# Kernel tuning notes

Hardware: AMD Instinct MI355X
Metric: run time of the kernel (lower is better)

Reference implementation:

```python
import jax, jax.numpy as jnp
import numpy as np

HIDDEN = 256

def _segment_mean(src, seg_ids, num_segments):
    # scatter_mean with count clamped to min 1 (matches torch reference)
    s = jax.ops.segment_sum(src, seg_ids, num_segments=num_segments)
    cnt = jax.ops.segment_sum(jnp.ones((src.shape[0],), src.dtype), seg_ids,
                              num_segments=num_segments)
    return s / jnp.maximum(cnt, 1.0)[:, None]


def setup_inputs() -> dict:
    key = jax.random.key(0)
    ks = jax.random.split(key, 12)
    N, E = 25000, 400000
    F_NODE, F_EDGE, F_OUT = 128, 128, 128
    x = jax.random.normal(ks[0], (N, F_NODE), jnp.float32)
    edge_index = jax.random.randint(ks[1], (2, E), 0, N, jnp.int64)
    edge_attr = jax.random.normal(ks[2], (E, F_EDGE), jnp.float32)
    u = jax.random.normal(ks[3], (1, 64), jnp.float32)
    batch = jnp.zeros((N,), jnp.int64)
    s1 = 1.0 / np.sqrt(F_NODE + F_EDGE)
    s2 = 1.0 / np.sqrt(HIDDEN)
    s3 = 1.0 / np.sqrt(F_NODE + HIDDEN)
    # node_mlp_1: Linear(256,256) -> ELU -> Linear(256,256)
    W1a = jax.random.uniform(ks[4], (F_NODE + F_EDGE, HIDDEN), jnp.float32, -s1, s1)
    b1a = jax.random.uniform(ks[5], (HIDDEN,), jnp.float32, -s1, s1)
    W1b = jax.random.uniform(ks[6], (HIDDEN, HIDDEN), jnp.float32, -s2, s2)
    b1b = jax.random.uniform(ks[7], (HIDDEN,), jnp.float32, -s2, s2)
    # node_mlp_2: Linear(384,256) -> ELU -> Linear(256,128)
    W2a = jax.random.uniform(ks[8], (F_NODE + HIDDEN, HIDDEN), jnp.float32, -s3, s3)
    b2a = jax.random.uniform(ks[9], (HIDDEN,), jnp.float32, -s3, s3)
    W2b = jax.random.uniform(ks[10], (HIDDEN, F_OUT), jnp.float32, -s2, s2)
    b2b = jax.random.uniform(ks[11], (F_OUT,), jnp.float32, -s2, s2)
    return {"x": x, "edge_index": edge_index, "edge_attr": edge_attr, "u": u,
            "batch": batch, "W1a": W1a, "b1a": b1a, "W1b": W1b, "b1b": b1b,
            "W2a": W2a, "b2a": b2a, "W2b": W2b, "b2b": b2b}


def reference(x, edge_index, edge_attr, u, batch,
              W1a, b1a, W1b, b1b, W2a, b2a, W2b, b2b):
    row, col = edge_index[0], edge_index[1]
    # gather source node feats per edge, concat with edge feats: [E, 256]
    h = jnp.concatenate([x[row], edge_attr], axis=1)
    # node_mlp_1
    h = jax.nn.elu(h @ W1a + b1a) @ W1b + b1b          # [E, 256]
    # scatter_mean onto destination nodes
    agg = _segment_mean(h, col, x.shape[0])             # [N, 256]
    # node_mlp_2 on [x, agg]
    z = jnp.concatenate([x, agg], axis=1)               # [N, 384]
    return jax.nn.elu(z @ W2a + b2a) @ W2b + b2b        # [N, 128]
```

## Files before the change

kernel.cpp:

```cpp
#include <hip/hip_runtime.h>
#include <hip/hip_bf16.h>
#include <stdint.h>

typedef short short8 __attribute__((ext_vector_type(8)));
typedef float f32x4 __attribute__((ext_vector_type(4)));
typedef float fvec4 __attribute__((ext_vector_type(4)));
typedef unsigned short us4 __attribute__((ext_vector_type(4)));

static __device__ __forceinline__ unsigned short f2bf(float f) {
  return __bfloat16_as_ushort(__float2bfloat16(f));
}

static __device__ __forceinline__ float bf2f(unsigned short u) {
  union { uint32_t u; float f; } v; v.u = (uint32_t)u << 16;
  return v.f;
}

static __device__ __forceinline__ float elu_f(float v) {
  return v > 0.0f ? v : __expf(v) - 1.0f;
}

__global__ void prep_kernel(const float* __restrict__ W1a, const float* __restrict__ W1b,
                            const float* __restrict__ W2a, const float* __restrict__ W2b,
                            unsigned short* __restrict__ w1aP, unsigned short* __restrict__ w1bP,
                            unsigned short* __restrict__ w2aP, unsigned short* __restrict__ w2bP,
                            const int* __restrict__ col_idx, int* __restrict__ cnt, int E,
                            float* __restrict__ agg, int aggN, int hb) {
  int b = blockIdx.x;
  if (b < 1024) {
    int p = b * 256 + threadIdx.x;
    const float* W; unsigned short* dst; int KT, Nc, q;
    if (p < 65536)       { W = W1a; dst = w1aP; KT = 8;  Nc = 256; q = p; }
    else if (p < 131072) { W = W1b; dst = w1bP; KT = 8;  Nc = 256; q = p - 65536; }
    else if (p < 229376) { W = W2a; dst = w2aP; KT = 12; Nc = 256; q = p - 131072; }
    else                 { W = W2b; dst = w2bP; KT = 8;  Nc = 128; q = p - 229376; }
    int i = q & 7;
    int l = (q >> 3) & 63;
    int rest = q >> 9;
    int kt = rest % KT;
    int nt = rest / KT;
    dst[q] = f2bf(W[(size_t)(kt * 32 + (l >> 4) * 8 + i) * Nc + nt * 16 + (l & 15)]);
  } else if (b < 1024 + hb) {
    int i = (b - 1024) * 256 + threadIdx.x;
    if (i < E) atomicAdd(&cnt[col_idx[i]], 1);
  } else {
    int idx = (b - 1024 - hb) * 256 + threadIdx.x;
    if (idx * 4 < aggN) {
      fvec4 z = {0.f, 0.f, 0.f, 0.f};
      *(fvec4*)(agg + (size_t)idx * 4) = z;
    }
  }
}

__global__ __launch_bounds__(1024) void scan_kernel(const int* __restrict__ cnt,
                                                    int* __restrict__ startA,
                                                    int* __restrict__ offs, int N, int E) {
  __shared__ int partial[1024];
  const int t = threadIdx.x;
  const int chunk = (N + 1023) >> 10;
  const int base = t * chunk;
  int s = 0;
  for (int i = 0; i < chunk; ++i) {
    int idx = base + i;
    if (idx < N) s += cnt[idx];
  }
  partial[t] = s;
  __syncthreads();
  for (int o = 1; o < 1024; o <<= 1) {
    int a = (t >= o) ? partial[t - o] : 0;
    __syncthreads();
    partial[t] += a;
    __syncthreads();
  }
  int run = partial[t] - s;
  for (int i = 0; i < chunk; ++i) {
    int idx = base + i;
    if (idx < N) {
      startA[idx] = run;
      offs[idx] = run;
      run += cnt[idx];
    }
  }
  if (t == 0) startA[N] = E;
}

__global__ void eid_kernel(const int* __restrict__ col_idx, int* __restrict__ offs,
                           int* __restrict__ eid, int E) {
  int i = blockIdx.x * blockDim.x + threadIdx.x;
  if (i < E) eid[atomicAdd(&offs[col_idx[i]], 1)] = i;
}

#define LDA 264
#define EBR 32

__global__ __launch_bounds__(256, 6) void edge_mlp_kernel(
    const float* __restrict__ x, const int* __restrict__ row_idx,
    const int* __restrict__ col_idx, const float* __restrict__ eattr,
    const float* __restrict__ b1a,
    const unsigned short* __restrict__ w1aP,
    const int* __restrict__ eid, float* __restrict__ agg) {
  __shared__ __align__(16) unsigned short As[EBR * LDA];
  __shared__ int rowi[EBR];
  __shared__ int eidx[EBR];
  __shared__ int dsts[EBR];
  const int t = threadIdx.x;
  const int e0 = blockIdx.x * EBR;

  if (t < EBR) {
    int e = eid[e0 + t];
    eidx[t] = e;
    rowi[t] = row_idx[e];
    dsts[t] = col_idx[e];
  }

  const int w = t >> 6, l = t & 63;
  const int lr = l & 15, lk = l >> 4;
  const unsigned short* B1 = w1aP + (size_t)(w * 32) * 512 + (size_t)l * 8;

  short8 bA[4], bB[4];
#pragma unroll
  for (int n = 0; n < 4; ++n) bA[n] = *(const short8*)(B1 + n * 4096);

  __syncthreads();

  for (int idx = t; idx < EBR * 64; idx += 256) {
    int e = idx >> 6, c4 = idx & 63;
    fvec4 v;
    if (c4 < 32)
      v = *(const fvec4*)(x + (size_t)rowi[e] * 128 + c4 * 4);
    else
      v = __builtin_nontemporal_load((const fvec4*)(eattr + (size_t)eidx[e] * 128 + (c4 - 32) * 4));
    us4 o;
    o.x = f2bf(v.x); o.y = f2bf(v.y); o.z = f2bf(v.z); o.w = f2bf(v.w);
    *(us4*)(&As[e * LDA + c4 * 4]) = o;
  }
  __syncthreads();

  f32x4 acc[2][4];
  const f32x4 zero4 = {0.f, 0.f, 0.f, 0.f};
#pragma unroll
  for (int mt = 0; mt < 2; ++mt)
#pragma unroll
    for (int nt = 0; nt < 4; ++nt) acc[mt][nt] = zero4;

#pragma unroll
  for (int kt = 0; kt < 8; ++kt) {
    short8* bc = (kt & 1) ? bB : bA;
    short8* bn = (kt & 1) ? bA : bB;
    if (kt < 7) {
#pragma unroll
      for (int n = 0; n < 4; ++n) bn[n] = *(const short8*)(B1 + n * 4096 + (kt + 1) * 512);
    }
    short8 a[2];
#pragma unroll
    for (int mt = 0; mt < 2; ++mt)
      a[mt] = *(const short8*)(&As[(mt * 16 + lr) * LDA + kt * 32 + lk * 8]);
#pragma unroll
    for (int mt = 0; mt < 2; ++mt)
#pragma unroll
      for (int nt = 0; nt < 4; ++nt)
        acc[mt][nt] = __builtin_amdgcn_mfma_f32_16x16x32_bf16(a[mt], bc[nt], acc[mt][nt], 0, 0, 0);
  }
  __syncthreads();

#pragma unroll
  for (int nt = 0; nt < 4; ++nt) {
    int col = w * 64 + nt * 16 + lr;
    float bias = b1a[col];
#pragma unroll
    for (int mt = 0; mt < 2; ++mt)
#pragma unroll
      for (int j = 0; j < 4; ++j) {
        float v = elu_f(acc[mt][nt][j] + bias);
        As[(mt * 16 + lk * 4 + j) * LDA + col] = f2bf(v);
      }
  }
  __syncthreads();

  {
    const int col = t;
    float run = 0.f;
    int prev = dsts[0];
    int segstart = 0;
#pragma unroll 8
    for (int r = 0; r < EBR; ++r) {
      int d = dsts[r];
      if (d != prev) {
        if (segstart == 0)
          atomicAdd(&agg[(size_t)prev * 256 + col], run);
        else
          agg[(size_t)prev * 256 + col] = run;
        run = 0.f;
        prev = d;
        segstart = r;
      }
      run += bf2f(As[r * LDA + col]);
    }
    atomicAdd(&agg[(size_t)prev * 256 + col], run);
  }
}

#define LDN 392

__global__ __launch_bounds__(256, 3) void node_mlp_kernel(
    const float* __restrict__ x, const float* __restrict__ agg,
    const int* __restrict__ startA, const float* __restrict__ b1b,
    const float* __restrict__ b2a, const float* __restrict__ b2b,
    const unsigned short* __restrict__ w1bP, const unsigned short* __restrict__ w2aP,
    const unsigned short* __restrict__ w2bP,
    float* __restrict__ out, int N) {
  __shared__ __align__(16) unsigned short As[64 * LDN];
  __shared__ float inv64[64];
  const int t = threadIdx.x;
  const int n0 = blockIdx.x * 64;

  const int w = t >> 6, l = t & 63;
  const int lr = l & 15, lk = l >> 4;
  const unsigned short* B0 = w1bP + (size_t)(w * 32) * 512 + (size_t)l * 8;
  const unsigned short* B1 = w2aP + (size_t)(w * 48) * 512 + (size_t)l * 8;
  const unsigned short* B2 = w2bP + (size_t)(w * 16) * 512 + (size_t)l * 8;

  if (t < 64) {
    int node = n0 + t;
    int cn = (node < N) ? (startA[node + 1] - startA[node]) : 0;
    inv64[t] = cn > 0 ? 1.0f / (float)cn : 0.f;
  }

  short8 bA[4], bB[4];
#pragma unroll
  for (int n = 0; n < 4; ++n) bA[n] = *(const short8*)(B0 + n * 4096);

  __syncthreads();

  for (int idx = t; idx < 64 * 64; idx += 256) {
    int nn = idx >> 6, c4 = idx & 63;
    int node = n0 + nn;
    fvec4 v = {0.f, 0.f, 0.f, 0.f};
    if (node < N) {
      float inv = inv64[nn];
      fvec4 a = *(const fvec4*)(agg + (size_t)node * 256 + c4 * 4);
      v.x = a.x * inv; v.y = a.y * inv; v.z = a.z * inv; v.w = a.w * inv;
    }
    us4 o;
    o.x = f2bf(v.x); o.y = f2bf(v.y); o.z = f2bf(v.z); o.w = f2bf(v.w);
    *(us4*)(&As[nn * 264 + c4 * 4]) = o;
  }
  __syncthreads();

  const f32x4 zero4 = {0.f, 0.f, 0.f, 0.f};
  f32x4 accU[4][4];
#pragma unroll
  for (int mt = 0; mt < 4; ++mt)
#pragma unroll
    for (int nt = 0; nt < 4; ++nt) accU[mt][nt] = zero4;

#pragma unroll
  for (int kt = 0; kt < 8; ++kt) {
    short8* bc = (kt & 1) ? bB : bA;
    short8* bn = (kt & 1) ? bA : bB;
    if (kt < 7) {
#pragma unroll
      for (int n = 0; n < 4; ++n) bn[n] = *(const short8*)(B0 + n * 4096 + (kt + 1) * 512);
    }
    short8 a[4];
#pragma unroll
    for (int mt = 0; mt < 4; ++mt)
      a[mt] = *(const short8*)(&As[(mt * 16 + lr) * 264 + kt * 32 + lk * 8]);
#pragma unroll
    for (int mt = 0; mt < 4; ++mt)
#pragma unroll
      for (int nt = 0; nt < 4; ++nt)
        accU[mt][nt] = __builtin_amdgcn_mfma_f32_16x16x32_bf16(a[mt], bc[nt], accU[mt][nt], 0, 0, 0);
  }

#pragma unroll
  for (int n = 0; n < 4; ++n) bA[n] = *(const short8*)(B1 + n * 6144);

  __syncthreads();

  for (int idx = t; idx < 64 * 32; idx += 256) {
    int nn = idx >> 5, c4 = idx & 31;
    int node = n0 + nn;
    fvec4 v = {0.f, 0.f, 0.f, 0.f};
    if (node < N) v = *(const fvec4*)(x + (size_t)node * 128 + c4 * 4);
    us4 o;
    o.x = f2bf(v.x); o.y = f2bf(v.y); o.z = f2bf(v.z); o.w = f2bf(v.w);
    *(us4*)(&As[nn * LDN + c4 * 4]) = o;
  }

#pragma unroll
  for (int nt = 0; nt < 4; ++nt) {
    int col = w * 64 + nt * 16 + lr;
    float bias = b1b[col];
#pragma unroll
    for (int mt = 0; mt < 4; ++mt)
#pragma unroll
      for (int j = 0; j < 4; ++j) {
        int row = mt * 16 + lk * 4 + j;
        float g = inv64[row] > 0.f ? 1.f : 0.f;
        As[row * LDN + 128 + col] = f2bf(accU[mt][nt][j] + g * bias);
      }
  }
  __syncthreads();

  f32x4 acc[4][4];
#pragma unroll
  for (int mt = 0; mt < 4; ++mt)
#pragma unroll
    for (int nt = 0; nt < 4; ++nt) acc[mt][nt] = zero4;

#pragma unroll
  for (int kt = 0; kt < 12; ++kt) {
    short8* bc = (kt & 1) ? bB : bA;
    short8* bn = (kt & 1) ? bA : bB;
    if (kt < 11) {
#pragma unroll
      for (int n = 0; n < 4; ++n) bn[n] = *(const short8*)(B1 + n * 6144 + (kt + 1) * 512);
    }
    short8 a[4];
#pragma unroll
    for (int mt = 0; mt < 4; ++mt)
      a[mt] = *(const short8*)(&As[(mt * 16 + lr) * LDN + kt * 32 + lk * 8]);
#pragma unroll
    for (int mt = 0; mt < 4; ++mt)
#pragma unroll
      for (int nt = 0; nt < 4; ++nt)
        acc[mt][nt] = __builtin_amdgcn_mfma_f32_16x16x32_bf16(a[mt], bc[nt], acc[mt][nt], 0, 0, 0);
  }

#pragma unroll
  for (int n = 0; n < 2; ++n) bA[n] = *(const short8*)(B2 + n * 4096);

  __syncthreads();

#pragma unroll
  for (int nt = 0; nt < 4; ++nt) {
    int col = w * 64 + nt * 16 + lr;
    float bias = b2a[col];
#pragma unroll
    for (int mt = 0; mt < 4; ++mt)
#pragma unroll
      for (int j = 0; j < 4; ++j) {
        float v = elu_f(acc[mt][nt][j] + bias);
        As[(mt * 16 + lk * 4 + j) * 264 + col] = f2bf(v);
      }
  }
  __syncthreads();

  f32x4 acc2[4][2];
#pragma unroll
  for (int mt = 0; mt < 4; ++mt)
#pragma unroll
    for (int nt = 0; nt < 2; ++nt) acc2[mt][nt] = zero4;
#pragma unroll
  for (int kt = 0; kt < 8; ++kt) {
    short8* bc = (kt & 1) ? bB : bA;
    short8* bn = (kt & 1) ? bA : bB;
    if (kt < 7) {
#pragma unroll
      for (int n = 0; n < 2; ++n) bn[n] = *(const short8*)(B2 + n * 4096 + (kt + 1) * 512);
    }
    short8 a[4];
#pragma unroll
    for (int mt = 0; mt < 4; ++mt)
      a[mt] = *(const short8*)(&As[(mt * 16 + lr) * 264 + kt * 32 + lk * 8]);
#pragma unroll
    for (int mt = 0; mt < 4; ++mt)
#pragma unroll
      for (int nt = 0; nt < 2; ++nt)
        acc2[mt][nt] = __builtin_amdgcn_mfma_f32_16x16x32_bf16(a[mt], bc[nt], acc2[mt][nt], 0, 0, 0);
  }

#pragma unroll
  for (int nt = 0; nt < 2; ++nt) {
    int col = w * 32 + nt * 16 + lr;
    float bias = b2b[col];
#pragma unroll
    for (int mt = 0; mt < 4; ++mt)
#pragma unroll
      for (int j = 0; j < 4; ++j) {
        int node = n0 + mt * 16 + lk * 4 + j;
        if (node < N) out[(size_t)node * 128 + col] = acc2[mt][nt][j] + bias;
      }
  }
}

extern "C" void kernel_launch(void* const* d_in, const int* in_sizes, int n_in,
                              void* d_out, int out_size, void* d_ws, size_t ws_size,
                              hipStream_t stream) {
  const float* x = (const float*)d_in[0];
  const int* ei = (const int*)d_in[1];
  const float* eattr = (const float*)d_in[2];
  const float* W1a = (const float*)d_in[5];
  const float* b1a = (const float*)d_in[6];
  const float* W1b = (const float*)d_in[7];
  const float* b1b = (const float*)d_in[8];
  const float* W2a = (const float*)d_in[9];
  const float* b2a = (const float*)d_in[10];
  const float* W2b = (const float*)d_in[11];
  const float* b2b = (const float*)d_in[12];

  const int N = in_sizes[0] / 128;
  const int E = in_sizes[2] / 128;

  char* ws = (char*)d_ws;
  float* agg = (float*)ws;
  size_t off = (size_t)N * 256 * 4;
  int* cntbuf = (int*)(ws + off); off += (size_t)N * 4;
  int* startA = (int*)(ws + off); off += (size_t)(N + 1) * 4;
  int* offs   = (int*)(ws + off); off += (size_t)N * 4;
  int* eid    = (int*)(ws + off); off += (size_t)E * 4;
  off = (off + 255) & ~(size_t)255;
  unsigned short* w1aP = (unsigned short*)(ws + off); off += 256 * 256 * 2;
  unsigned short* w1bP = (unsigned short*)(ws + off); off += 256 * 256 * 2;
  unsigned short* w2aP = (unsigned short*)(ws + off); off += 384 * 256 * 2;
  unsigned short* w2bP = (unsigned short*)(ws + off);

  (void)hipMemsetAsync(cntbuf, 0, (size_t)N * 4, stream);

  const int hb = (E + 255) / 256;
  const int aggN = N * 256;
  const int zb = (aggN / 4 + 255) / 256;

  prep_kernel<<<1024 + hb + zb, 256, 0, stream>>>(
      W1a, W1b, W2a, W2b, w1aP, w1bP, w2aP, w2bP, ei + E, cntbuf, E, agg, aggN, hb);

  scan_kernel<<<1, 1024, 0, stream>>>(cntbuf, startA, offs, N, E);
  eid_kernel<<<hb, 256, 0, stream>>>(ei + E, offs, eid, E);

  edge_mlp_kernel<<<E / EBR, 256, 0, stream>>>(x, ei, ei + E, eattr, b1a, w1aP, eid, agg);

  node_mlp_kernel<<<(N + 63) / 64, 256, 0, stream>>>(x, agg, startA, b1b, b2a, b2b,
                                                     w1bP, w2aP, w2bP, (float*)d_out, N);
}
```

Before: 260.8 us.

## Pre-sort edge attributes to bf16 in CSR order and pre-convert x to bf16

The eid permutation kernel is replaced by a scatter kernel that writes row/dst indices and bf16-converted edge attributes directly into destination-sorted order. x is converted to bf16 once in the prep kernel. The edge MLP then reads contiguous bf16 edge rows and half-size x rows with no conversion and no eid indirection. The cost is an extra full write and read of a bf16 copy of edge_attr (about 100MB) in exchange for a random fp32 gather that no longer has to happen inside the MLP kernel.

```diff
diff --git a/kernel.cpp b/kernel.cpp
--- a/kernel.cpp
+++ b/kernel.cpp
@@ -6,6 +6,7 @@
 typedef float f32x4 __attribute__((ext_vector_type(4)));
 typedef float fvec4 __attribute__((ext_vector_type(4)));
 typedef unsigned short us4 __attribute__((ext_vector_type(4)));
+typedef unsigned short us8 __attribute__((ext_vector_type(8)));
 
 static __device__ __forceinline__ unsigned short f2bf(float f) {
   return __bfloat16_as_ushort(__float2bfloat16(f));
@@ -25,7 +26,9 @@
                             unsigned short* __restrict__ w1aP, unsigned short* __restrict__ w1bP,
                             unsigned short* __restrict__ w2aP, unsigned short* __restrict__ w2bP,
                             const int* __restrict__ col_idx, int* __restrict__ cnt, int E,
-                            float* __restrict__ agg, int aggN, int hb) {
+                            float* __restrict__ agg, int aggN, int hb, int zb,
+                            const float* __restrict__ x, unsigned short* __restrict__ xH,
+                            int xElems) {
   int b = blockIdx.x;
   if (b < 1024) {
     int p = b * 256 + threadIdx.x;
@@ -43,11 +46,22 @@
   } else if (b < 1024 + hb) {
     int i = (b - 1024) * 256 + threadIdx.x;
     if (i < E) atomicAdd(&cnt[col_idx[i]], 1);
-  } else {
+  } else if (b < 1024 + hb + zb) {
     int idx = (b - 1024 - hb) * 256 + threadIdx.x;
     if (idx * 4 < aggN) {
       fvec4 z = {0.f, 0.f, 0.f, 0.f};
       *(fvec4*)(agg + (size_t)idx * 4) = z;
+    }
+  } else {
+    int idx = (b - 1024 - hb - zb) * 256 + threadIdx.x;
+    if (idx * 8 < xElems) {
+      const float* src = x + (size_t)idx * 8;
+      fvec4 a = *(const fvec4*)src;
+      fvec4 c = *(const fvec4*)(src + 4);
+      us8 o;
+      o[0] = f2bf(a.x); o[1] = f2bf(a.y); o[2] = f2bf(a.z); o[3] = f2bf(a.w);
+      o[4] = f2bf(c.x); o[5] = f2bf(c.y); o[6] = f2bf(c.z); o[7] = f2bf(c.w);
+      *(us8*)(xH + (size_t)idx * 8) = o;
     }
   }
 }
@@ -84,33 +98,54 @@
   if (t == 0) startA[N] = E;
 }
 
-__global__ void eid_kernel(const int* __restrict__ col_idx, int* __restrict__ offs,
-                           int* __restrict__ eid, int E) {
-  int i = blockIdx.x * blockDim.x + threadIdx.x;
-  if (i < E) eid[atomicAdd(&offs[col_idx[i]], 1)] = i;
+__global__ __launch_bounds__(256) void scatter_kernel(
+    const int* __restrict__ row_idx, const int* __restrict__ col_idx,
+    const float* __restrict__ eattr, int* __restrict__ offs,
+    int* __restrict__ rowS, int* __restrict__ dstS,
+    unsigned short* __restrict__ eattrS, int E) {
+  __shared__ int rr[64];
+  const int t = threadIdx.x;
+  const int e0 = blockIdx.x * 64;
+
+  if (t < 64) {
+    int e = e0 + t;
+    int d = col_idx[e];
+    int r = atomicAdd(&offs[d], 1);
+    rr[t] = r;
+    rowS[r] = row_idx[e];
+    dstS[r] = d;
+  }
+  __syncthreads();
+
+  for (int idx = t; idx < 64 * 16; idx += 256) {
+    int e = idx >> 4, c = idx & 15;
+    const fvec4* src = (const fvec4*)(eattr + (size_t)(e0 + e) * 128 + c * 8);
+    fvec4 a = __builtin_nontemporal_load(src);
+    fvec4 b = __builtin_nontemporal_load(src + 1);
+    us8 o;
+    o[0] = f2bf(a.x); o[1] = f2bf(a.y); o[2] = f2bf(a.z); o[3] = f2bf(a.w);
+    o[4] = f2bf(b.x); o[5] = f2bf(b.y); o[6] = f2bf(b.z); o[7] = f2bf(b.w);
+    *(us8*)(eattrS + (size_t)rr[e] * 128 + c * 8) = o;
+  }
 }
 
 #define LDA 264
 #define EBR 32
 
 __global__ __launch_bounds__(256, 6) void edge_mlp_kernel(
-    const float* __restrict__ x, const int* __restrict__ row_idx,
-    const int* __restrict__ col_idx, const float* __restrict__ eattr,
-    const float* __restrict__ b1a,
-    const unsigned short* __restrict__ w1aP,
-    const int* __restrict__ eid, float* __restrict__ agg) {
+    const unsigned short* __restrict__ xH, const int* __restrict__ rowS,
+    const int* __restrict__ dstS, const unsigned short* __restrict__ eattrS,
+    const float* __restrict__ b1a, const unsigned short* __restrict__ w1aP,
+    float* __restrict__ agg) {
   __shared__ __align__(16) unsigned short As[EBR * LDA];
   __shared__ int rowi[EBR];
-  __shared__ int eidx[EBR];
   __shared__ int dsts[EBR];
   const int t = threadIdx.x;
   const int e0 = blockIdx.x * EBR;
 
   if (t < EBR) {
-    int e = eid[e0 + t];
-    eidx[t] = e;
-    rowi[t] = row_idx[e];
-    dsts[t] = col_idx[e];
+    rowi[t] = rowS[e0 + t];
+    dsts[t] = dstS[e0 + t];
   }
 
   const int w = t >> 6, l = t & 63;
@@ -123,16 +158,14 @@
 
   __syncthreads();
 
-  for (int idx = t; idx < EBR * 64; idx += 256) {
-    int e = idx >> 6, c4 = idx & 63;
-    fvec4 v;
-    if (c4 < 32)
-      v = *(const fvec4*)(x + (size_t)rowi[e] * 128 + c4 * 4);
+  for (int idx = t; idx < EBR * 32; idx += 256) {
+    int e = idx >> 5, g = idx & 31;
+    us8 v;
+    if (g < 16)
+      v = *(const us8*)(xH + (size_t)rowi[e] * 128 + g * 8);
     else
-      v = __builtin_nontemporal_load((const fvec4*)(eattr + (size_t)eidx[e] * 128 + (c4 - 32) * 4));
-    us4 o;
-    o.x = f2bf(v.x); o.y = f2bf(v.y); o.z = f2bf(v.z); o.w = f2bf(v.w);
-    *(us4*)(&As[e * LDA + c4 * 4]) = o;
+      v = *(const us8*)(eattrS + (size_t)(e0 + e) * 128 + (g - 16) * 8);
+    *(us8*)(&As[e * LDA + g * 8]) = v;
   }
   __syncthreads();
 
@@ -409,8 +442,12 @@
   int* cntbuf = (int*)(ws + off); off += (size_t)N * 4;
   int* startA = (int*)(ws + off); off += (size_t)(N + 1) * 4;
   int* offs   = (int*)(ws + off); off += (size_t)N * 4;
-  int* eid    = (int*)(ws + off); off += (size_t)E * 4;
+  int* rowS   = (int*)(ws + off); off += (size_t)E * 4;
+  int* dstS   = (int*)(ws + off); off += (size_t)E * 4;
   off = (off + 255) & ~(size_t)255;
+  unsigned short* xH     = (unsigned short*)(ws + off); off += (size_t)N * 128 * 2;
+  off = (off + 255) & ~(size_t)255;
+  unsigned short* eattrS = (unsigned short*)(ws + off); off += (size_t)E * 128 * 2;
   unsigned short* w1aP = (unsigned short*)(ws + off); off += 256 * 256 * 2;
   unsigned short* w1bP = (unsigned short*)(ws + off); off += 256 * 256 * 2;
   unsigned short* w2aP = (unsigned short*)(ws + off); off += 384 * 256 * 2;
@@ -421,14 +458,19 @@
   const int hb = (E + 255) / 256;
   const int aggN = N * 256;
   const int zb = (aggN / 4 + 255) / 256;
-
-  prep_kernel<<<1024 + hb + zb, 256, 0, stream>>>(
-      W1a, W1b, W2a, W2b, w1aP, w1bP, w2aP, w2bP, ei + E, cntbuf, E, agg, aggN, hb);
+  const int xElems = N * 128;
+  const int xb = (xElems / 8 + 255) / 256;
+
+  prep_kernel<<<1024 + hb + zb + xb, 256, 0, stream>>>(
+      W1a, W1b, W2a, W2b, w1aP, w1bP, w2aP, w2bP, ei + E, cntbuf, E,
+      agg, aggN, hb, zb, x, xH, xElems);
 
   scan_kernel<<<1, 1024, 0, stream>>>(cntbuf, startA, offs, N, E);
-  eid_kernel<<<hb, 256, 0, stream>>>(ei + E, offs, eid, E);
-
-  edge_mlp_kernel<<<E / EBR, 256, 0, stream>>>(x, ei, ei + E, eattr, b1a, w1aP, eid, agg);
+
+  scatter_kernel<<<E / 64, 256, 0, stream>>>(ei, ei + E, eattr, offs,
+                                             rowS, dstS, eattrS, E);
+
+  edge_mlp_kernel<<<E / EBR, 256, 0, stream>>>(xH, rowS, dstS, eattrS, b1a, w1aP, agg);
 
   node_mlp_kernel<<<(N + 63) / 64, 256, 0, stream>>>(x, agg, startA, b1b, b2a, b2b,
                                                      w1bP, w2aP, w2bP, (float*)d_out, N);
```

Result: slower. 279.7 us (+7.3%).

## Fuse edge MLP, segment mean and node MLP into one node-tiled kernel

Applied to the files above, without the earlier changes.

Replaces the separate edge-MLP and node-MLP kernels with one kernel in which each block owns 32 destination nodes and walks their CSR-sorted incoming edges in chunks. Segment sums accumulate in LDS rather than through global atomics into an fp32 agg buffer, which removes the agg zeroing, the atomics and the agg round trip through global memory. x is converted to bf16 once in the prep kernel so the gathers read half as many bytes. The trade-off is imbalance: blocks whose nodes have many incoming edges take longer. Larger LDS use per block and the smaller node tile for the node MLP can also lower occupancy and weight reuse.

```diff
diff --git a/kernel.cpp b/kernel.cpp
--- a/kernel.cpp
+++ b/kernel.cpp
@@ -6,6 +6,7 @@
 typedef float f32x4 __attribute__((ext_vector_type(4)));
 typedef float fvec4 __attribute__((ext_vector_type(4)));
 typedef unsigned short us4 __attribute__((ext_vector_type(4)));
+typedef unsigned short us8 __attribute__((ext_vector_type(8)));
 
 static __device__ __forceinline__ unsigned short f2bf(float f) {
   return __bfloat16_as_ushort(__float2bfloat16(f));
@@ -25,7 +26,8 @@
                             unsigned short* __restrict__ w1aP, unsigned short* __restrict__ w1bP,
                             unsigned short* __restrict__ w2aP, unsigned short* __restrict__ w2bP,
                             const int* __restrict__ col_idx, int* __restrict__ cnt, int E,
-                            float* __restrict__ agg, int aggN, int hb) {
+                            int hb, const float* __restrict__ x,
+                            unsigned short* __restrict__ xH, int xElems) {
   int b = blockIdx.x;
   if (b < 1024) {
     int p = b * 256 + threadIdx.x;
@@ -45,9 +47,14 @@
     if (i < E) atomicAdd(&cnt[col_idx[i]], 1);
   } else {
     int idx = (b - 1024 - hb) * 256 + threadIdx.x;
-    if (idx * 4 < aggN) {
-      fvec4 z = {0.f, 0.f, 0.f, 0.f};
-      *(fvec4*)(agg + (size_t)idx * 4) = z;
+    if (idx * 8 < xElems) {
+      const float* src = x + (size_t)idx * 8;
+      fvec4 a = *(const fvec4*)src;
+      fvec4 c = *(const fvec4*)(src + 4);
+      us8 o;
+      o[0] = f2bf(a.x); o[1] = f2bf(a.y); o[2] = f2bf(a.z); o[3] = f2bf(a.w);
+      o[4] = f2bf(c.x); o[5] = f2bf(c.y); o[6] = f2bf(c.z); o[7] = f2bf(c.w);
+      *(us8*)(xH + (size_t)idx * 8) = o;
     }
   }
 }
@@ -91,82 +98,237 @@
 }
 
 #define LDA 264
-#define EBR 32
-
-__global__ __launch_bounds__(256, 6) void edge_mlp_kernel(
-    const float* __restrict__ x, const int* __restrict__ row_idx,
-    const int* __restrict__ col_idx, const float* __restrict__ eattr,
-    const float* __restrict__ b1a,
-    const unsigned short* __restrict__ w1aP,
-    const int* __restrict__ eid, float* __restrict__ agg) {
-  __shared__ __align__(16) unsigned short As[EBR * LDA];
-  __shared__ int rowi[EBR];
-  __shared__ int eidx[EBR];
-  __shared__ int dsts[EBR];
+#define LDX 392
+#define LDC 260
+#define NBF 32
+
+__global__ __launch_bounds__(256, 3) void fused_kernel(
+    const unsigned short* __restrict__ xH, const int* __restrict__ eid,
+    const int* __restrict__ row_idx, const float* __restrict__ eattr,
+    const int* __restrict__ startA,
+    const float* __restrict__ b1a, const float* __restrict__ b1b,
+    const float* __restrict__ b2a, const float* __restrict__ b2b,
+    const unsigned short* __restrict__ w1aP, const unsigned short* __restrict__ w1bP,
+    const unsigned short* __restrict__ w2aP, const unsigned short* __restrict__ w2bP,
+    float* __restrict__ out, int N) {
+  __shared__ __align__(16) float accumS[NBF * LDC];
+  __shared__ __align__(16) unsigned short As[NBF * LDA];
+  __shared__ int startL[NBF + 1];
+  __shared__ int eidL[NBF], rowiL[NBF], nodeL[NBF];
+  __shared__ float invL[NBF];
+
   const int t = threadIdx.x;
-  const int e0 = blockIdx.x * EBR;
-
-  if (t < EBR) {
-    int e = eid[e0 + t];
-    eidx[t] = e;
-    rowi[t] = row_idx[e];
-    dsts[t] = col_idx[e];
-  }
-
+  const int n0 = blockIdx.x * NBF;
   const int w = t >> 6, l = t & 63;
   const int lr = l & 15, lk = l >> 4;
-  const unsigned short* B1 = w1aP + (size_t)(w * 32) * 512 + (size_t)l * 8;
-
+
+  if (t < NBF + 1) startL[t] = startA[min(n0 + t, N)];
+  for (int idx = t; idx < NBF * 256; idx += 256)
+    accumS[(idx >> 8) * LDC + (idx & 255)] = 0.f;
+  __syncthreads();
+  if (t < NBF) {
+    int cn = startL[t + 1] - startL[t];
+    invL[t] = cn > 0 ? 1.0f / (float)cn : 0.f;
+  }
+  const int sBase = startL[0], sEnd = startL[NBF];
+
+  const unsigned short* B1w = w1aP + (size_t)(w * 32) * 512 + (size_t)l * 8;
   short8 bA[4], bB[4];
-#pragma unroll
-  for (int n = 0; n < 4; ++n) bA[n] = *(const short8*)(B1 + n * 4096);
-
-  __syncthreads();
-
-  for (int idx = t; idx < EBR * 64; idx += 256) {
-    int e = idx >> 6, c4 = idx & 63;
-    fvec4 v;
-    if (c4 < 32)
-      v = *(const fvec4*)(x + (size_t)rowi[e] * 128 + c4 * 4);
-    else
-      v = __builtin_nontemporal_load((const fvec4*)(eattr + (size_t)eidx[e] * 128 + (c4 - 32) * 4));
-    us4 o;
-    o.x = f2bf(v.x); o.y = f2bf(v.y); o.z = f2bf(v.z); o.w = f2bf(v.w);
-    *(us4*)(&As[e * LDA + c4 * 4]) = o;
-  }
-  __syncthreads();
-
   f32x4 acc[2][4];
   const f32x4 zero4 = {0.f, 0.f, 0.f, 0.f};
+
+  float biasA[4];
+#pragma unroll
+  for (int nt = 0; nt < 4; ++nt) biasA[nt] = b1a[w * 64 + nt * 16 + lr];
+
+  for (int s = sBase; s < sEnd; s += NBF) {
+    __syncthreads();
+    if (t < NBF) {
+      int slot = s + t;
+      int sl = slot < sEnd ? slot : sEnd - 1;
+      int e = eid[sl];
+      eidL[t] = e;
+      rowiL[t] = row_idx[e];
+      int lo = 0;
+#pragma unroll
+      for (int st = 16; st > 0; st >>= 1)
+        if (lo + st <= NBF - 1 && startL[lo + st] <= sl) lo += st;
+      nodeL[t] = lo;
+    }
+#pragma unroll
+    for (int n = 0; n < 4; ++n) bA[n] = *(const short8*)(B1w + n * 4096);
+    __syncthreads();
+
+    for (int idx = t; idx < NBF * 32; idx += 256) {
+      int r = idx >> 5, g = idx & 31;
+      us8 v;
+      if (g < 16) {
+        v = *(const us8*)(xH + (size_t)rowiL[r] * 128 + g * 8);
+      } else {
+        const fvec4* src = (const fvec4*)(eattr + (size_t)eidL[r] * 128 + (size_t)(g - 16) * 8);
+        fvec4 a = __builtin_nontemporal_load(src);
+        fvec4 b = __builtin_nontemporal_load(src + 1);
+        v[0] = f2bf(a.x); v[1] = f2bf(a.y); v[2] = f2bf(a.z); v[3] = f2bf(a.w);
+        v[4] = f2bf(b.x); v[5] = f2bf(b.y); v[6] = f2bf(b.z); v[7] = f2bf(b.w);
+      }
+      *(us8*)(&As[r * LDA + g * 8]) = v;
+    }
+    __syncthreads();
+
+#pragma unroll
+    for (int mt = 0; mt < 2; ++mt)
+#pragma unroll
+      for (int nt = 0; nt < 4; ++nt) acc[mt][nt] = zero4;
+#pragma unroll
+    for (int kt = 0; kt < 8; ++kt) {
+      short8* bc = (kt & 1) ? bB : bA;
+      short8* bn = (kt & 1) ? bA : bB;
+      if (kt < 7) {
+#pragma unroll
+        for (int n = 0; n < 4; ++n) bn[n] = *(const short8*)(B1w + n * 4096 + (kt + 1) * 512);
+      }
+      short8 a[2];
+#pragma unroll
+      for (int mt = 0; mt < 2; ++mt)
+        a[mt] = *(const short8*)(&As[(mt * 16 + lr) * LDA + kt * 32 + lk * 8]);
+#pragma unroll
+      for (int mt = 0; mt < 2; ++mt)
+#pragma unroll
+        for (int nt = 0; nt < 4; ++nt)
+          acc[mt][nt] = __builtin_amdgcn_mfma_f32_16x16x32_bf16(a[mt], bc[nt], acc[mt][nt], 0, 0, 0);
+    }
+    __syncthreads();
+
+#pragma unroll
+    for (int nt = 0; nt < 4; ++nt) {
+      int col = w * 64 + nt * 16 + lr;
+#pragma unroll
+      for (int mt = 0; mt < 2; ++mt)
+#pragma unroll
+        for (int j = 0; j < 4; ++j) {
+          float v = elu_f(acc[mt][nt][j] + biasA[nt]);
+          As[(mt * 16 + lk * 4 + j) * LDA + col] = f2bf(v);
+        }
+    }
+    __syncthreads();
+
+    {
+      int c = sEnd - s; if (c > NBF) c = NBF;
+      const int col = t;
+      float run = 0.f;
+      int prev = nodeL[0];
+      for (int r = 0; r < c; ++r) {
+        int nd = nodeL[r];
+        if (nd != prev) { accumS[prev * LDC + col] += run; run = 0.f; prev = nd; }
+        run += bf2f(As[r * LDA + col]);
+      }
+      accumS[prev * LDC + col] += run;
+    }
+  }
+  __syncthreads();
+
+  const unsigned short* B0  = w1bP + (size_t)(w * 32) * 512 + (size_t)l * 8;
+  const unsigned short* B1n = w2aP + (size_t)(w * 48) * 512 + (size_t)l * 8;
+  const unsigned short* B2n = w2bP + (size_t)(w * 16) * 512 + (size_t)l * 8;
+
+#pragma unroll
+  for (int n = 0; n < 4; ++n) bA[n] = *(const short8*)(B0 + n * 4096);
+
+  for (int idx = t; idx < NBF * 64; idx += 256) {
+    int nn = idx >> 6, c4 = idx & 63;
+    float inv = invL[nn];
+    const float* a = &accumS[nn * LDC + c4 * 4];
+    us4 o;
+    o.x = f2bf(a[0] * inv); o.y = f2bf(a[1] * inv);
+    o.z = f2bf(a[2] * inv); o.w = f2bf(a[3] * inv);
+    *(us4*)(&As[nn * LDA + c4 * 4]) = o;
+  }
+  __syncthreads();
+
+  f32x4 accU[2][4];
 #pragma unroll
   for (int mt = 0; mt < 2; ++mt)
 #pragma unroll
-    for (int nt = 0; nt < 4; ++nt) acc[mt][nt] = zero4;
-
+    for (int nt = 0; nt < 4; ++nt) accU[mt][nt] = zero4;
 #pragma unroll
   for (int kt = 0; kt < 8; ++kt) {
     short8* bc = (kt & 1) ? bB : bA;
     short8* bn = (kt & 1) ? bA : bB;
     if (kt < 7) {
 #pragma unroll
-      for (int n = 0; n < 4; ++n) bn[n] = *(const short8*)(B1 + n * 4096 + (kt + 1) * 512);
+      for (int n = 0; n < 4; ++n) bn[n] = *(const short8*)(B0 + n * 4096 + (kt + 1) * 512);
     }
     short8 a[2];
 #pragma unroll
     for (int mt = 0; mt < 2; ++mt)
       a[mt] = *(const short8*)(&As[(mt * 16 + lr) * LDA + kt * 32 + lk * 8]);
+#pragma unroll
+    for (int mt = 0; mt < 2; ++mt)
+#pragma unroll
+      for (int nt = 0; nt < 4; ++nt)
+        accU[mt][nt] = __builtin_amdgcn_mfma_f32_16x16x32_bf16(a[mt], bc[nt], accU[mt][nt], 0, 0, 0);
+  }
+
+  unsigned short* XB = (unsigned short*)accumS;
+
+  for (int idx = t; idx < NBF * 16; idx += 256) {
+    int nn = idx >> 4, g = idx & 15;
+    int node = n0 + nn;
+    us8 v = {0, 0, 0, 0, 0, 0, 0, 0};
+    if (node < N) v = *(const us8*)(xH + (size_t)node * 128 + g * 8);
+    *(us8*)(&XB[nn * LDX + g * 8]) = v;
+  }
+
+#pragma unroll
+  for (int n = 0; n < 4; ++n) bA[n] = *(const short8*)(B1n + n * 6144);
+
+#pragma unroll
+  for (int nt = 0; nt < 4; ++nt) {
+    int col = w * 64 + nt * 16 + lr;
+    float bias = b1b[col];
+#pragma unroll
+    for (int mt = 0; mt < 2; ++mt)
+#pragma unroll
+      for (int j = 0; j < 4; ++j) {
+        int row = mt * 16 + lk * 4 + j;
+        float g = invL[row] > 0.f ? 1.f : 0.f;
+        XB[row * LDX + 128 + col] = f2bf(accU[mt][nt][j] + g * bias);
+      }
+  }
+  __syncthreads();
+
+#pragma unroll
+  for (int mt = 0; mt < 2; ++mt)
+#pragma unroll
+    for (int nt = 0; nt < 4; ++nt) acc[mt][nt] = zero4;
+#pragma unroll
+  for (int kt = 0; kt < 12; ++kt) {
+    short8* bc = (kt & 1) ? bB : bA;
+    short8* bn = (kt & 1) ? bA : bB;
+    if (kt < 11) {
+#pragma unroll
+      for (int n = 0; n < 4; ++n) bn[n] = *(const short8*)(B1n + n * 6144 + (kt + 1) * 512);
+    }
+    short8 a[2];
+#pragma unroll
+    for (int mt = 0; mt < 2; ++mt)
+      a[mt] = *(const short8*)(&XB[(mt * 16 + lr) * LDX + kt * 32 + lk * 8]);
 #pragma unroll
     for (int mt = 0; mt < 2; ++mt)
 #pragma unroll
       for (int nt = 0; nt < 4; ++nt)
         acc[mt][nt] = __builtin_amdgcn_mfma_f32_16x16x32_bf16(a[mt], bc[nt], acc[mt][nt], 0, 0, 0);
   }
+
+#pragma unroll
+  for (int n = 0; n < 2; ++n) bA[n] = *(const short8*)(B2n + n * 4096);
+
   __syncthreads();
 
 #pragma unroll
   for (int nt = 0; nt < 4; ++nt) {
     int col = w * 64 + nt * 16 + lr;
-    float bias = b1a[col];
+    float bias = b2a[col];
 #pragma unroll
     for (int mt = 0; mt < 2; ++mt)
 #pragma unroll
@@ -177,195 +339,25 @@
   }
   __syncthreads();
 
-  {
-    const int col = t;
-    float run = 0.f;
-    int prev = dsts[0];
-    int segstart = 0;
-#pragma unroll 8
-    for (int r = 0; r < EBR; ++r) {
-      int d = dsts[r];
-      if (d != prev) {
-        if (segstart == 0)
-          atomicAdd(&agg[(size_t)prev * 256 + col], run);
-        else
-          agg[(size_t)prev * 256 + col] = run;
-        run = 0.f;
-        prev = d;
-        segstart = r;
-      }
-      run += bf2f(As[r * LDA + col]);
-    }
-    atomicAdd(&agg[(size_t)prev * 256 + col], run);
-  }
-}
-
-#define LDN 392
-
-__global__ __launch_bounds__(256, 3) void node_mlp_kernel(
-    const float* __restrict__ x, const float* __restrict__ agg,
-    const int* __restrict__ startA, const float* __restrict__ b1b,
-    const float* __restrict__ b2a, const float* __restrict__ b2b,
-    const unsigned short* __restrict__ w1bP, const unsigned short* __restrict__ w2aP,
-    const unsigned short* __restrict__ w2bP,
-    float* __restrict__ out, int N) {
-  __shared__ __align__(16) unsigned short As[64 * LDN];
-  __shared__ float inv64[64];
-  const int t = threadIdx.x;
-  const int n0 = blockIdx.x * 64;
-
-  const int w = t >> 6, l = t & 63;
-  const int lr = l & 15, lk = l >> 4;
-  const unsigned short* B0 = w1bP + (size_t)(w * 32) * 512 + (size_t)l * 8;
-  const unsigned short* B1 = w2aP + (size_t)(w * 48) * 512 + (size_t)l * 8;
-  const unsigned short* B2 = w2bP + (size_t)(w * 16) * 512 + (size_t)l * 8;
-
-  if (t < 64) {
-    int node = n0 + t;
-    int cn = (node < N) ? (startA[node + 1] - startA[node]) : 0;
-    inv64[t] = cn > 0 ? 1.0f / (float)cn : 0.f;
-  }
-
-  short8 bA[4], bB[4];
-#pragma unroll
-  for (int n = 0; n < 4; ++n) bA[n] = *(const short8*)(B0 + n * 4096);
-
-  __syncthreads();
-
-  for (int idx = t; idx < 64 * 64; idx += 256) {
-    int nn = idx >> 6, c4 = idx & 63;
-    int node = n0 + nn;
-    fvec4 v = {0.f, 0.f, 0.f, 0.f};
-    if (node < N) {
-      float inv = inv64[nn];
-      fvec4 a = *(const fvec4*)(agg + (size_t)node * 256 + c4 * 4);
-      v.x = a.x * inv; v.y = a.y * inv; v.z = a.z * inv; v.w = a.w * inv;
-    }
-    us4 o;
-    o.x = f2bf(v.x); o.y = f2bf(v.y); o.z = f2bf(v.z); o.w = f2bf(v.w);
-    *(us4*)(&As[nn * 264 + c4 * 4]) = o;
-  }
-  __syncthreads();
-
-  const f32x4 zero4 = {0.f, 0.f, 0.f, 0.f};
-  f32x4 accU[4][4];
-#pragma unroll
-  for (int mt = 0; mt < 4; ++mt)
-#pragma unroll
-    for (int nt = 0; nt < 4; ++nt) accU[mt][nt] = zero4;
-
+  f32x4 acc2[2][2];
+#pragma unroll
+  for (int mt = 0; mt < 2; ++mt)
+#pragma unroll
+    for (int nt = 0; nt < 2; ++nt) acc2[mt][nt] = zero4;
 #pragma unroll
   for (int kt = 0; kt < 8; ++kt) {
     short8* bc = (kt & 1) ? bB : bA;
     short8* bn = (kt & 1) ? bA : bB;
     if (kt < 7) {
 #pragma unroll
-      for (int n = 0; n < 4; ++n) bn[n] = *(const short8*)(B0 + n * 4096 + (kt + 1) * 512);
-    }
-    short8 a[4];
-#pragma unroll
-    for (int mt = 0; mt < 4; ++mt)
-      a[mt] = *(const short8*)(&As[(mt * 16 + lr) * 264 + kt * 32 + lk * 8]);
-#pragma unroll
-    for (int mt = 0; mt < 4; ++mt)
-#pragma unroll
-      for (int nt = 0; nt < 4; ++nt)
-        accU[mt][nt] = __builtin_amdgcn_mfma_f32_16x16x32_bf16(a[mt], bc[nt], accU[mt][nt], 0, 0, 0);
-  }
-
-#pragma unroll
-  for (int n = 0; n < 4; ++n) bA[n] = *(const short8*)(B1 + n * 6144);
-
-  __syncthreads();
-
-  for (int idx = t; idx < 64 * 32; idx += 256) {
-    int nn = idx >> 5, c4 = idx & 31;
-    int node = n0 + nn;
-    fvec4 v = {0.f, 0.f, 0.f, 0.f};
-    if (node < N) v = *(const fvec4*)(x + (size_t)node * 128 + c4 * 4);
-    us4 o;
-    o.x = f2bf(v.x); o.y = f2bf(v.y); o.z = f2bf(v.z); o.w = f2bf(v.w);
-    *(us4*)(&As[nn * LDN + c4 * 4]) = o;
-  }
-
-#pragma unroll
-  for (int nt = 0; nt < 4; ++nt) {
-    int col = w * 64 + nt * 16 + lr;
-    float bias = b1b[col];
-#pragma unroll
-    for (int mt = 0; mt < 4; ++mt)
-#pragma unroll
-      for (int j = 0; j < 4; ++j) {
-        int row = mt * 16 + lk * 4 + j;
-        float g = inv64[row] > 0.f ? 1.f : 0.f;
-        As[row * LDN + 128 + col] = f2bf(accU[mt][nt][j] + g * bias);
-      }
-  }
-  __syncthreads();
-
-  f32x4 acc[4][4];
-#pragma unroll
-  for (int mt = 0; mt < 4; ++mt)
-#pragma unroll
-    for (int nt = 0; nt < 4; ++nt) acc[mt][nt] = zero4;
-
-#pragma unroll
-  for (int kt = 0; kt < 12; ++kt) {
-    short8* bc = (kt & 1) ? bB : bA;
-    short8* bn = (kt & 1) ? bA : bB;
-    if (kt < 11) {
-#pragma unroll
-      for (int n = 0; n < 4; ++n) bn[n] = *(const short8*)(B1 + n * 6144 + (kt + 1) * 512);
-    }
-    short8 a[4];
-#pragma unroll
-    for (int mt = 0; mt < 4; ++mt)
-      a[mt] = *(const short8*)(&As[(mt * 16 + lr) * LDN + kt * 32 + lk * 8]);
-#pragma unroll
-    for (int mt = 0; mt < 4; ++mt)
-#pragma unroll
-      for (int nt = 0; nt < 4; ++nt)
-        acc[mt][nt] = __builtin_amdgcn_mfma_f32_16x16x32_bf16(a[mt], bc[nt], acc[mt][nt], 0, 0, 0);
-  }
-
-#pragma unroll
-  for (int n = 0; n < 2; ++n) bA[n] = *(const short8*)(B2 + n * 4096);
-
-  __syncthreads();
-
-#pragma unroll
-  for (int nt = 0; nt < 4; ++nt) {
-    int col = w * 64 + nt * 16 + lr;
-    float bias = b2a[col];
-#pragma unroll
-    for (int mt = 0; mt < 4; ++mt)
-#pragma unroll
-      for (int j = 0; j < 4; ++j) {
-        float v = elu_f(acc[mt][nt][j] + bias);
-        As[(mt * 16 + lk * 4 + j) * 264 + col] = f2bf(v);
-      }
-  }
-  __syncthreads();
-
-  f32x4 acc2[4][2];
-#pragma unroll
-  for (int mt = 0; mt < 4; ++mt)
-#pragma unroll
-    for (int nt = 0; nt < 2; ++nt) acc2[mt][nt] = zero4;
-#pragma unroll
-  for (int kt = 0; kt < 8; ++kt) {
-    short8* bc = (kt & 1) ? bB : bA;
-    short8* bn = (kt & 1) ? bA : bB;
-    if (kt < 7) {
-#pragma unroll
-      for (int n = 0; n < 2; ++n) bn[n] = *(const short8*)(B2 + n * 4096 + (kt + 1) * 512);
-    }
-    short8 a[4];
-#pragma unroll
-    for (int mt = 0; mt < 4; ++mt)
-      a[mt] = *(const short8*)(&As[(mt * 16 + lr) * 264 + kt * 32 + lk * 8]);
-#pragma unroll
-    for (int mt = 0; mt < 4; ++mt)
+      for (int n = 0; n < 2; ++n) bn[n] = *(const short8*)(B2n + n * 4096 + (kt + 1) * 512);
+    }
+    short8 a[2];
+#pragma unroll
+    for (int mt = 0; mt < 2; ++mt)
+      a[mt] = *(const short8*)(&As[(mt * 16 + lr) * LDA + kt * 32 + lk * 8]);
+#pragma unroll
+    for (int mt = 0; mt < 2; ++mt)
 #pragma unroll
       for (int nt = 0; nt < 2; ++nt)
         acc2[mt][nt] = __builtin_amdgcn_mfma_f32_16x16x32_bf16(a[mt], bc[nt], acc2[mt][nt], 0, 0, 0);
@@ -376,7 +368,7 @@
     int col = w * 32 + nt * 16 + lr;
     float bias = b2b[col];
 #pragma unroll
-    for (int mt = 0; mt < 4; ++mt)
+    for (int mt = 0; mt < 2; ++mt)
 #pragma unroll
       for (int j = 0; j < 4; ++j) {
         int node = n0 + mt * 16 + lk * 4 + j;
@@ -404,13 +396,13 @@
   const int E = in_sizes[2] / 128;
 
   char* ws = (char*)d_ws;
-  float* agg = (float*)ws;
-  size_t off = (size_t)N * 256 * 4;
+  size_t off = 0;
   int* cntbuf = (int*)(ws + off); off += (size_t)N * 4;
   int* startA = (int*)(ws + off); off += (size_t)(N + 1) * 4;
   int* offs   = (int*)(ws + off); off += (size_t)N * 4;
   int* eid    = (int*)(ws + off); off += (size_t)E * 4;
   off = (off + 255) & ~(size_t)255;
+  unsigned short* xH   = (unsigned short*)(ws + off); off += (size_t)N * 128 * 2;
   unsigned short* w1aP = (unsigned short*)(ws + off); off += 256 * 256 * 2;
   unsigned short* w1bP = (unsigned short*)(ws + off); off += 256 * 256 * 2;
   unsigned short* w2aP = (unsigned short*)(ws + off); off += 384 * 256 * 2;
@@ -419,17 +411,16 @@
   (void)hipMemsetAsync(cntbuf, 0, (size_t)N * 4, stream);
 
   const int hb = (E + 255) / 256;
-  const int aggN = N * 256;
-  const int zb = (aggN / 4 + 255) / 256;
-
-  prep_kernel<<<1024 + hb + zb, 256, 0, stream>>>(
-      W1a, W1b, W2a, W2b, w1aP, w1bP, w2aP, w2bP, ei + E, cntbuf, E, agg, aggN, hb);
+  const int xElems = N * 128;
+  const int xb = (xElems / 8 + 255) / 256;
+
+  prep_kernel<<<1024 + hb + xb, 256, 0, stream>>>(
+      W1a, W1b, W2a, W2b, w1aP, w1bP, w2aP, w2bP, ei + E, cntbuf, E, hb, x, xH, xElems);
 
   scan_kernel<<<1, 1024, 0, stream>>>(cntbuf, startA, offs, N, E);
   eid_kernel<<<hb, 256, 0, stream>>>(ei + E, offs, eid, E);
 
-  edge_mlp_kernel<<<E / EBR, 256, 0, stream>>>(x, ei, ei + E, eattr, b1a, w1aP, eid, agg);
-
-  node_mlp_kernel<<<(N + 63) / 64, 256, 0, stream>>>(x, agg, startA, b1b, b2a, b2b,
-                                                     w1bP, w2aP, w2bP, (float*)d_out, N);
-}
+  fused_kernel<<<(N + NBF - 1) / NBF, 256, 0, stream>>>(
+      xH, eid, ei, eattr, startA, b1a, b1b, b2a, b2b,
+      w1aP, w1bP, w2aP, w2bP, (float*)d_out, N);
+}
```

Result: slower. 452.6 us (+73.6%).

## Pre-convert x to bf16 and gather edge inputs directly into registers

Applied to the files above, without the earlier changes.

The prep kernel now also converts node features x to a bf16 copy, so the edge kernel gathers half as many bytes per source node. The edge kernel drops the shared-memory index staging and its first barrier: each thread loads its edge id, gathers 8-element bf16 vectors of x or converts edge_attr, and writes them straight to the shared A tile. This removes a synchronisation and the dependent index round-trip through shared memory. The cost is an extra workspace buffer and an extra pass over x in the prep kernel.

```diff
diff --git a/kernel.cpp b/kernel.cpp
--- a/kernel.cpp
+++ b/kernel.cpp
@@ -6,6 +6,7 @@
 typedef float f32x4 __attribute__((ext_vector_type(4)));
 typedef float fvec4 __attribute__((ext_vector_type(4)));
 typedef unsigned short us4 __attribute__((ext_vector_type(4)));
+typedef unsigned short us8 __attribute__((ext_vector_type(8)));
 
 static __device__ __forceinline__ unsigned short f2bf(float f) {
   return __bfloat16_as_ushort(__float2bfloat16(f));
@@ -25,7 +26,9 @@
                             unsigned short* __restrict__ w1aP, unsigned short* __restrict__ w1bP,
                             unsigned short* __restrict__ w2aP, unsigned short* __restrict__ w2bP,
                             const int* __restrict__ col_idx, int* __restrict__ cnt, int E,
-                            float* __restrict__ agg, int aggN, int hb) {
+                            int hb, const float* __restrict__ x,
+                            unsigned short* __restrict__ xH, int xElems,
+                            float* __restrict__ agg, int aggN) {
   int b = blockIdx.x;
   if (b < 1024) {
     int p = b * 256 + threadIdx.x;
@@ -45,6 +48,15 @@
     if (i < E) atomicAdd(&cnt[col_idx[i]], 1);
   } else {
     int idx = (b - 1024 - hb) * 256 + threadIdx.x;
+    if (idx * 8 < xElems) {
+      const float* src = x + (size_t)idx * 8;
+      fvec4 a = *(const fvec4*)src;
+      fvec4 c = *(const fvec4*)(src + 4);
+      us8 o;
+      o[0] = f2bf(a.x); o[1] = f2bf(a.y); o[2] = f2bf(a.z); o[3] = f2bf(a.w);
+      o[4] = f2bf(c.x); o[5] = f2bf(c.y); o[6] = f2bf(c.z); o[7] = f2bf(c.w);
+      *(us8*)(xH + (size_t)idx * 8) = o;
+    }
     if (idx * 4 < aggN) {
       fvec4 z = {0.f, 0.f, 0.f, 0.f};
       *(fvec4*)(agg + (size_t)idx * 4) = z;
@@ -94,24 +106,37 @@
 #define EBR 32
 
 __global__ __launch_bounds__(256, 6) void edge_mlp_kernel(
-    const float* __restrict__ x, const int* __restrict__ row_idx,
+    const unsigned short* __restrict__ xH, const int* __restrict__ row_idx,
     const int* __restrict__ col_idx, const float* __restrict__ eattr,
-    const float* __restrict__ b1a,
-    const unsigned short* __restrict__ w1aP,
+    const float* __restrict__ b1a, const unsigned short* __restrict__ w1aP,
     const int* __restrict__ eid, float* __restrict__ agg) {
   __shared__ __align__(16) unsigned short As[EBR * LDA];
-  __shared__ int rowi[EBR];
-  __shared__ int eidx[EBR];
   __shared__ int dsts[EBR];
   const int t = threadIdx.x;
   const int e0 = blockIdx.x * EBR;
 
-  if (t < EBR) {
-    int e = eid[e0 + t];
-    eidx[t] = e;
-    rowi[t] = row_idx[e];
-    dsts[t] = col_idx[e];
-  }
+  const int r = t >> 3;
+  const int g0 = (t & 7) << 2;
+
+  int e = eid[e0 + r];
+
+  us8 v[4];
+  if (g0 < 16) {
+    int row = row_idx[e];
+    const us8* src = (const us8*)(xH + (size_t)row * 128 + (size_t)g0 * 8);
+#pragma unroll
+    for (int i = 0; i < 4; ++i) v[i] = src[i];
+  } else {
+    const fvec4* src = (const fvec4*)(eattr + (size_t)e * 128 + (size_t)(g0 - 16) * 8);
+#pragma unroll
+    for (int i = 0; i < 4; ++i) {
+      fvec4 a = __builtin_nontemporal_load(src + 2 * i);
+      fvec4 b = __builtin_nontemporal_load(src + 2 * i + 1);
+      v[i][0] = f2bf(a.x); v[i][1] = f2bf(a.y); v[i][2] = f2bf(a.z); v[i][3] = f2bf(a.w);
+      v[i][4] = f2bf(b.x); v[i][5] = f2bf(b.y); v[i][6] = f2bf(b.z); v[i][7] = f2bf(b.w);
+    }
+  }
+  if ((t & 7) == 0) dsts[r] = col_idx[e];
 
   const int w = t >> 6, l = t & 63;
   const int lr = l & 15, lk = l >> 4;
@@ -121,19 +146,9 @@
 #pragma unroll
   for (int n = 0; n < 4; ++n) bA[n] = *(const short8*)(B1 + n * 4096);
 
-  __syncthreads();
-
-  for (int idx = t; idx < EBR * 64; idx += 256) {
-    int e = idx >> 6, c4 = idx & 63;
-    fvec4 v;
-    if (c4 < 32)
-      v = *(const fvec4*)(x + (size_t)rowi[e] * 128 + c4 * 4);
-    else
-      v = __builtin_nontemporal_load((const fvec4*)(eattr + (size_t)eidx[e] * 128 + (c4 - 32) * 4));
-    us4 o;
-    o.x = f2bf(v.x); o.y = f2bf(v.y); o.z = f2bf(v.z); o.w = f2bf(v.w);
-    *(us4*)(&As[e * LDA + c4 * 4]) = o;
-  }
+#pragma unroll
+  for (int i = 0; i < 4; ++i)
+    *(us8*)(&As[r * LDA + (g0 + i) * 8]) = v[i];
   __syncthreads();
 
   f32x4 acc[2][4];
@@ -171,8 +186,8 @@
     for (int mt = 0; mt < 2; ++mt)
 #pragma unroll
       for (int j = 0; j < 4; ++j) {
-        float v = elu_f(acc[mt][nt][j] + bias);
-        As[(mt * 16 + lk * 4 + j) * LDA + col] = f2bf(v);
+        float vv = elu_f(acc[mt][nt][j] + bias);
+        As[(mt * 16 + lk * 4 + j) * LDA + col] = f2bf(vv);
       }
   }
   __syncthreads();
@@ -183,8 +198,8 @@
     int prev = dsts[0];
     int segstart = 0;
 #pragma unroll 8
-    for (int r = 0; r < EBR; ++r) {
-      int d = dsts[r];
+    for (int rr = 0; rr < EBR; ++rr) {
+      int d = dsts[rr];
       if (d != prev) {
         if (segstart == 0)
           atomicAdd(&agg[(size_t)prev * 256 + col], run);
@@ -192,9 +207,9 @@
           agg[(size_t)prev * 256 + col] = run;
         run = 0.f;
         prev = d;
-        segstart = r;
+        segstart = rr;
       }
-      run += bf2f(As[r * LDA + col]);
+      run += bf2f(As[rr * LDA + col]);
     }
     atomicAdd(&agg[(size_t)prev * 256 + col], run);
   }
@@ -411,6 +426,7 @@
   int* offs   = (int*)(ws + off); off += (size_t)N * 4;
   int* eid    = (int*)(ws + off); off += (size_t)E * 4;
   off = (off + 255) & ~(size_t)255;
+  unsigned short* xH   = (unsigned short*)(ws + off); off += (size_t)N * 128 * 2;
   unsigned short* w1aP = (unsigned short*)(ws + off); off += 256 * 256 * 2;
   unsigned short* w1bP = (unsigned short*)(ws + off); off += 256 * 256 * 2;
   unsigned short* w2aP = (unsigned short*)(ws + off); off += 384 * 256 * 2;
@@ -419,16 +435,19 @@
   (void)hipMemsetAsync(cntbuf, 0, (size_t)N * 4, stream);
 
   const int hb = (E + 255) / 256;
+  const int xElems = N * 128;
   const int aggN = N * 256;
-  const int zb = (aggN / 4 + 255) / 256;
-
-  prep_kernel<<<1024 + hb + zb, 256, 0, stream>>>(
-      W1a, W1b, W2a, W2b, w1aP, w1bP, w2aP, w2bP, ei + E, cntbuf, E, agg, aggN, hb);
+  const int tail = (aggN / 4 > xElems / 8) ? aggN / 4 : xElems / 8;
+  const int xb = (tail + 255) / 256;
+
+  prep_kernel<<<1024 + hb + xb, 256, 0, stream>>>(
+      W1a, W1b, W2a, W2b, w1aP, w1bP, w2aP, w2bP, ei + E, cntbuf, E, hb,
+      x, xH, xElems, agg, aggN);
 
   scan_kernel<<<1, 1024, 0, stream>>>(cntbuf, startA, offs, N, E);
   eid_kernel<<<hb, 256, 0, stream>>>(ei + E, offs, eid, E);
 
-  edge_mlp_kernel<<<E / EBR, 256, 0, stream>>>(x, ei, ei + E, eattr, b1a, w1aP, eid, agg);
+  edge_mlp_kernel<<<E / EBR, 256, 0, stream>>>(xH, ei, ei + E, eattr, b1a, w1aP, eid, agg);
 
   node_mlp_kernel<<<(N + 63) / 64, 256, 0, stream>>>(x, agg, startA, b1b, b2a, b2b,
                                                      w1bP, w2aP, w2bP, (float*)d_out, N);
```

New measurement: 327.8 us. +25.7%, slower.
